# Kernel optimization log

Hardware: AMD Instinct MI355X
Metric: run time of the kernel (lower is better)

Reference implementation:

```python
import jax, jax.numpy as jnp
import numpy as np

N = 100000
E = 1600000
D = 64
EPS = 1e-5


def setup_inputs() -> dict:
    key = jax.random.key(0)
    ks = jax.random.split(key, 16)
    x = jax.random.normal(ks[0], (N, D), dtype=jnp.float32)
    edge_index = jax.random.randint(ks[1], (2, E), 0, N, dtype=jnp.int64)
    s = 1.0 / np.sqrt(D)
    params = {
        'W1': jax.random.uniform(ks[2], (D, D), jnp.float32, -s, s),
        'b1': jnp.zeros((D,), jnp.float32),
        'g1': jnp.ones((D,), jnp.float32),
        'be1': jnp.zeros((D,), jnp.float32),
        'W2': jax.random.uniform(ks[3], (D, D), jnp.float32, -s, s),
        'b2': jnp.zeros((D,), jnp.float32),
        'g2': jnp.ones((D,), jnp.float32),
        'be2': jnp.zeros((D,), jnp.float32),
        'W3': jax.random.uniform(ks[4], (D, D), jnp.float32, -s, s),
        'b3': jnp.zeros((D,), jnp.float32),
    }
    return {'x': x, 'edge_index': edge_index, **params}


def _gcn_norm(edge_index):
    # add self-loops, symmetric normalization (PyG GCNConv default)
    loop = jnp.arange(N, dtype=edge_index.dtype)
    src = jnp.concatenate([edge_index[0], loop])  # [E+N]
    dst = jnp.concatenate([edge_index[1], loop])
    deg = jax.ops.segment_sum(jnp.ones_like(src, dtype=jnp.float32), dst, num_segments=N)
    dinv = jnp.where(deg > 0, jax.lax.rsqrt(deg), 0.0)
    norm = dinv[src] * dinv[dst]  # [E+N]
    return src, dst, norm


def _gcn_conv(x, src, dst, norm, W, b):
    h = x @ W                        # [N, D] transform first (PyG order)
    msg = h[src] * norm[:, None]     # gather + scale  [E+N, D]
    out = jax.ops.segment_sum(msg, dst, num_segments=N)  # scatter-add
    return out + b


def _bn(x, g, b):
    # BatchNorm1d over nodes, batch statistics (training-mode math)
    m = jnp.mean(x, axis=0)
    v = jnp.var(x, axis=0)
    return g * (x - m) * jax.lax.rsqrt(v + EPS) + b


def reference(x, edge_index, W1, b1, g1, be1, W2, b2, g2, be2, W3, b3):
    src, dst, norm = _gcn_norm(edge_index)
    h = _gcn_conv(x, src, dst, norm, W1, b1)
    h = jax.nn.relu(_bn(h, g1, be1))
    h = _gcn_conv(h, src, dst, norm, W2, b2)
    h = jax.nn.relu(_bn(h, g2, be2))
    h = _gcn_conv(h, src, dst, norm, W3, b3)
    return h
```

## Files before the change

### kernel.cpp

```cpp
#include <hip/hip_runtime.h>
#include <hip/hip_bf16.h>


#define FD 64
#define EPSF 1e-5f

#define NBUCK 256
#define BSHIFT 9
#define BWID 512
#define SLOTS 28
#define P1_EDGES 4096
#define RPMASK 0x3FFFFF

typedef __attribute__((ext_vector_type(8))) short bf16x8;
typedef __attribute__((ext_vector_type(4))) float f32x4;

__device__ __forceinline__ ushort f2bf_bits(float f) {
  __hip_bfloat16 h = __float2bfloat16(f);
  return *(ushort*)&h;
}
__device__ __forceinline__ unsigned packbf(float lo, float hi) {
  return (unsigned)f2bf_bits(lo) | ((unsigned)f2bf_bits(hi) << 16);
}

__global__ __launch_bounds__(256) void init_kernel(int* __restrict__ bcur,
                                                   float* __restrict__ stats1,
                                                   float* __restrict__ stats2,
                                                   int nB, int cap) {
  int t = threadIdx.x;
  if (t < nB) bcur[t] = t * cap;
  if (t < 128) {
    stats1[t] = 0.f;
    stats2[t] = 0.f;
  }
}

__global__ __launch_bounds__(256) void fill1_kernel(const int* __restrict__ ei, int E,
                                                    int* __restrict__ bcur,
                                                    int2* __restrict__ stage) {
  __shared__ int2 sbuf[NBUCK][SLOTS];
  __shared__ int scnt[NBUCK];
  __shared__ int sbase[NBUCK];
  __shared__ int s_is64;
  const int tid = threadIdx.x;
  scnt[tid] = 0;
  if (tid < 64) {
    int v = ei[2 * tid + 1];
    unsigned long long nz = __ballot(v != 0);
    if (tid == 0) s_is64 = (nz == 0ull) ? 1 : 0;
  }
  __syncthreads();
  const int is64 = s_is64;
  const int base = blockIdx.x * P1_EDGES;
#pragma unroll 1
  for (int k = 0; k < P1_EDGES / 256; ++k) {
    int e = base + k * 256 + tid;
    if (e < E) {
      int s = is64 ? ei[2 * e] : ei[e];
      int d = is64 ? ei[2 * (E + e)] : ei[E + e];
      int b = d >> BSHIFT;
      int pos = atomicAdd(&scnt[b], 1);
      if (pos < SLOTS) {
        sbuf[b][pos] = make_int2(s, d);
      } else {
        stage[atomicAdd(&bcur[b], 1)] = make_int2(s, d);
      }
    }
  }
  __syncthreads();
  {
    int c = scnt[tid];
    if (c > SLOTS) c = SLOTS;
    scnt[tid] = c;
    sbase[tid] = c ? atomicAdd(&bcur[tid], c) : 0;
  }
  __syncthreads();
  for (int idx = tid; idx < NBUCK * SLOTS; idx += 256) {
    int b = idx / SLOTS, sl = idx - b * SLOTS;
    if (sl < scnt[b]) stage[sbase[b] + sl] = sbuf[b][sl];
  }
}

__global__ __launch_bounds__(256) void degscan_kernel(const int2* __restrict__ stage,
                                                      const int* __restrict__ bcur,
                                                      int* __restrict__ rowptr,
                                                      float* __restrict__ dinv,
                                                      int N, int cap) {
  __shared__ int h[BWID];
  __shared__ int ps[256];
  const int b = blockIdx.x;
  const int tid = threadIdx.x;
  h[tid] = 0;
  h[tid + 256] = 0;
  __syncthreads();
  const int lo = b * cap, hi = bcur[b];
  for (int i = lo + tid; i < hi; i += 256)
    atomicAdd(&h[stage[i].y - (b << BSHIFT)], 1);
  __syncthreads();
  const int a0 = h[2 * tid], a1 = h[2 * tid + 1];
  ps[tid] = a0 + a1;
  __syncthreads();
  for (int off = 1; off < 256; off <<= 1) {
    int v = (tid >= off) ? ps[tid - off] : 0;
    __syncthreads();
    ps[tid] += v;
    __syncthreads();
  }
  const int excl = ps[tid] - (a0 + a1);
  const int n0 = b << BSHIFT;
  const int na = n0 + 2 * tid;
  const int nb2 = na + 1;
  if (na < N) {
    rowptr[na] = (lo + excl) | (min(a0, 1023) << 22);
    dinv[na] = rsqrtf((float)(a0 + 1));
  }
  if (nb2 < N) {
    rowptr[nb2] = (lo + excl + a0) | (min(a1, 1023) << 22);
    dinv[nb2] = rsqrtf((float)(a1 + 1));
  }
}

__global__ __launch_bounds__(512) void fill2_kernel(const int2* __restrict__ stage,
                                                    const int* __restrict__ bcur,
                                                    const int* __restrict__ rowptr,
                                                    const float* __restrict__ dinv,
                                                    int2* __restrict__ colw, int N,
                                                    int cap) {
  __shared__ int lcur[BWID];
  const int b = blockIdx.x;
  const int tid = threadIdx.x;
  const int n0 = b << BSHIFT;
  if (tid < BWID) {
    int node = n0 + tid;
    lcur[tid] = (node < N) ? (rowptr[node] & RPMASK) : 0;
  }
  __syncthreads();
  const int lo = b * cap, hi = bcur[b];
  for (int i = lo + tid; i < hi; i += 512) {
    int2 sd = stage[i];
    int slot = atomicAdd(&lcur[sd.y - n0], 1);
    colw[slot] = make_int2(sd.x, __float_as_int(dinv[sd.x] * dinv[sd.y]));
  }
}

__global__ void detect64_kernel(const int* __restrict__ ei, int* __restrict__ flag) {
  int lane = threadIdx.x;
  int v = ei[2 * lane + 1];
  unsigned long long nz = __ballot(v != 0);
  if (lane == 0) *flag = (nz == 0ull) ? 1 : 0;
}
__global__ __launch_bounds__(256) void deg_atomic_kernel(const int* __restrict__ ei, int E,
                                                         const int* __restrict__ flag,
                                                         int* __restrict__ deg) {
  int e = blockIdx.x * 256 + threadIdx.x;
  if (e >= E) return;
  const int is64 = *flag;
  int d = is64 ? ei[2 * (E + e)] : ei[E + e];
  atomicAdd(&deg[d], 1);
}
__global__ __launch_bounds__(256) void dinv_kernel(const int* __restrict__ deg,
                                                   float* __restrict__ dinv, int N) {
  int i = blockIdx.x * 256 + threadIdx.x;
  if (i < N) dinv[i] = rsqrtf((float)(deg[i] + 1));
}
__global__ __launch_bounds__(1024) void scan1_kernel(const int* __restrict__ deg,
                                                     int* __restrict__ tmp,
                                                     int* __restrict__ partial, int N) {
  __shared__ int lds[1024];
  int i = blockIdx.x * 1024 + threadIdx.x;
  int v = (i < N) ? deg[i] : 0;
  lds[threadIdx.x] = v;
  __syncthreads();
  for (int off = 1; off < 1024; off <<= 1) {
    int t = (threadIdx.x >= (unsigned)off) ? lds[threadIdx.x - off] : 0;
    __syncthreads();
    lds[threadIdx.x] += t;
    __syncthreads();
  }
  if (i < N) tmp[i] = lds[threadIdx.x];
  if (threadIdx.x == 1023) partial[blockIdx.x] = lds[1023];
}
__global__ __launch_bounds__(128) void scan2_kernel(int* __restrict__ partial, int B) {
  __shared__ int lds[128];
  int t = threadIdx.x;
  int v = (t < B) ? partial[t] : 0;
  lds[t] = v;
  __syncthreads();
  for (int off = 1; off < 128; off <<= 1) {
    int tv = (t >= off) ? lds[t - off] : 0;
    __syncthreads();
    lds[t] += tv;
    __syncthreads();
  }
  if (t < B) partial[t] = lds[t] - v;
}
__global__ __launch_bounds__(1024) void scan3_kernel(const int* __restrict__ deg,
                                                     const int* __restrict__ tmp,
                                                     const int* __restrict__ partial,
                                                     int* __restrict__ rowptr,
                                                     int* __restrict__ cursor, int N) {
  int i = blockIdx.x * 1024 + threadIdx.x;
  if (i < N) {
    int d = deg[i];
    int start = tmp[i] + partial[blockIdx.x] - d;
    rowptr[i] = start | (min(d, 1023) << 22);
    cursor[i] = start;
  }
}
__global__ __launch_bounds__(256) void fill_direct_kernel(const int* __restrict__ ei, int E,
                                                          const int* __restrict__ flag,
                                                          const float* __restrict__ dinv,
                                                          int* __restrict__ cursor,
                                                          int2* __restrict__ colw) {
  int e = blockIdx.x * 256 + threadIdx.x;
  if (e >= E) return;
  const int is64 = *flag;
  int s = is64 ? ei[2 * e] : ei[e];
  int d = is64 ? ei[2 * (E + e)] : ei[E + e];
  int slot = atomicAdd(&cursor[d], 1);
  colw[slot] = make_int2(s, __float_as_int(dinv[s] * dinv[d]));
}

__global__ __launch_bounds__(256) void cast_kernel(const float* __restrict__ in,
                                                   ushort* __restrict__ out, int total) {
  int i = (blockIdx.x * 256 + threadIdx.x) * 4;
  if (i >= total) return;
  float4 v = *(const float4*)(in + i);
  ushort4 o;
  o.x = f2bf_bits(v.x);
  o.y = f2bf_bits(v.y);
  o.z = f2bf_bits(v.z);
  o.w = f2bf_bits(v.w);
  *(ushort4*)(out + i) = o;
}

__global__ __launch_bounds__(256) void bnrelu_kernel(ushort* __restrict__ T,
                                                     const float* __restrict__ stats,
                                                     const float* __restrict__ g,
                                                     const float* __restrict__ be,
                                                     int N) {
  __shared__ float sa[FD], sc[FD];
  if (threadIdx.x < FD) {
    const float invN = 1.0f / (float)N;
    float m = stats[threadIdx.x] * invN;
    float v = stats[FD + threadIdx.x] * invN - m * m;
    float r = rsqrtf(v + EPSF);
    float a = g[threadIdx.x] * r;
    sa[threadIdx.x] = a;
    sc[threadIdx.x] = be[threadIdx.x] - m * a;
  }
  __syncthreads();
  const int idx = (blockIdx.x * 256 + threadIdx.x) * 8;
  if (idx >= N * FD) return;
  const int f0 = idx & (FD - 1);
  uint4 v = *(const uint4*)(T + idx);
  float h0 = __uint_as_float(v.x << 16);
  float h1 = __uint_as_float(v.x & 0xffff0000u);
  float h2 = __uint_as_float(v.y << 16);
  float h3 = __uint_as_float(v.y & 0xffff0000u);
  float h4 = __uint_as_float(v.z << 16);
  float h5 = __uint_as_float(v.z & 0xffff0000u);
  float h6 = __uint_as_float(v.w << 16);
  float h7 = __uint_as_float(v.w & 0xffff0000u);
  h0 = fmaxf(fmaf(sa[f0 + 0], h0, sc[f0 + 0]), 0.f);
  h1 = fmaxf(fmaf(sa[f0 + 1], h1, sc[f0 + 1]), 0.f);
  h2 = fmaxf(fmaf(sa[f0 + 2], h2, sc[f0 + 2]), 0.f);
  h3 = fmaxf(fmaf(sa[f0 + 3], h3, sc[f0 + 3]), 0.f);
  h4 = fmaxf(fmaf(sa[f0 + 4], h4, sc[f0 + 4]), 0.f);
  h5 = fmaxf(fmaf(sa[f0 + 5], h5, sc[f0 + 5]), 0.f);
  h6 = fmaxf(fmaf(sa[f0 + 6], h6, sc[f0 + 6]), 0.f);
  h7 = fmaxf(fmaf(sa[f0 + 7], h7, sc[f0 + 7]), 0.f);
  uint4 o;
  o.x = packbf(h0, h1);
  o.y = packbf(h2, h3);
  o.z = packbf(h4, h5);
  o.w = packbf(h6, h7);
  *(uint4*)(T + idx) = o;
}

__global__ __launch_bounds__(256) void agg_kernel(const ushort* __restrict__ H,
                                                  const int* __restrict__ rowptr,
                                                  const int2* __restrict__ colw,
                                                  const float* __restrict__ dinv,
                                                  ushort* __restrict__ out, int N) {
  const int lane = threadIdx.x & 63;
  const int wid = threadIdx.x >> 6;
  const int grp = lane >> 4;
  const int sg = (lane >> 3) & 1;
  const int fl8 = lane & 7;
  const int dst = (blockIdx.x * 4 + wid) * 4 + grp;
  const bool live = dst < N;
  const int dc = live ? dst : N - 1;

  const unsigned rp = (unsigned)rowptr[dc];
  const int e0 = (int)(rp & RPMASK);
  const int e1 = live ? e0 + (int)(rp >> 22) : e0;

  float acc[4][8];
#pragma unroll
  for (int u = 0; u < 4; ++u)
#pragma unroll
    for (int j = 0; j < 8; ++j) acc[u][j] = 0.f;

  for (int base = e0; __any(base < e1); base += 8) {
#pragma unroll
    for (int u = 0; u < 4; ++u) {
      const int ee = base + 2 * u + sg;
      const bool valid = ee < e1;
      const int idx = valid ? ee : 0;
      const int2 cw = colw[idx];
      const float w = valid ? __int_as_float(cw.y) : 0.f;
      const uint4 uv = *(const uint4*)(H + (size_t)cw.x * FD + fl8 * 8);
      acc[u][0] = fmaf(w, __uint_as_float(uv.x << 16), acc[u][0]);
      acc[u][1] = fmaf(w, __uint_as_float(uv.x & 0xffff0000u), acc[u][1]);
      acc[u][2] = fmaf(w, __uint_as_float(uv.y << 16), acc[u][2]);
      acc[u][3] = fmaf(w, __uint_as_float(uv.y & 0xffff0000u), acc[u][3]);
      acc[u][4] = fmaf(w, __uint_as_float(uv.z << 16), acc[u][4]);
      acc[u][5] = fmaf(w, __uint_as_float(uv.z & 0xffff0000u), acc[u][5]);
      acc[u][6] = fmaf(w, __uint_as_float(uv.w << 16), acc[u][6]);
      acc[u][7] = fmaf(w, __uint_as_float(uv.w & 0xffff0000u), acc[u][7]);
    }
  }

  float r[8];
#pragma unroll
  for (int j = 0; j < 8; ++j)
    r[j] = (acc[0][j] + acc[1][j]) + (acc[2][j] + acc[3][j]);
#pragma unroll
  for (int j = 0; j < 8; ++j) r[j] += __shfl_xor(r[j], 8);

  const float di = dinv[dc];
  const float dsq = di * di;
  const uint4 sv = *(const uint4*)(H + (size_t)dc * FD + fl8 * 8);
  r[0] = fmaf(dsq, __uint_as_float(sv.x << 16), r[0]);
  r[1] = fmaf(dsq, __uint_as_float(sv.x & 0xffff0000u), r[1]);
  r[2] = fmaf(dsq, __uint_as_float(sv.y << 16), r[2]);
  r[3] = fmaf(dsq, __uint_as_float(sv.y & 0xffff0000u), r[3]);
  r[4] = fmaf(dsq, __uint_as_float(sv.z << 16), r[4]);
  r[5] = fmaf(dsq, __uint_as_float(sv.z & 0xffff0000u), r[5]);
  r[6] = fmaf(dsq, __uint_as_float(sv.w << 16), r[6]);
  r[7] = fmaf(dsq, __uint_as_float(sv.w & 0xffff0000u), r[7]);

  if (live && sg == 0) {
    uint4 o;
    o.x = packbf(r[0], r[1]);
    o.y = packbf(r[2], r[3]);
    o.z = packbf(r[4], r[5]);
    o.w = packbf(r[6], r[7]);
    *(uint4*)(out + (size_t)dst * FD + fl8 * 8) = o;
  }
}

template <bool BF16OUT>
__global__ __launch_bounds__(256) void gemm_mfma_kernel(const ushort* __restrict__ A,
                                                        const float* __restrict__ W,
                                                        const float* __restrict__ bias,
                                                        ushort* __restrict__ outb,
                                                        float* __restrict__ outf,
                                                        float* __restrict__ stats, int N) {
  const int lane = threadIdx.x & 63;
  const int wid = threadIdx.x >> 6;
  const int lo = lane & 15;
  const int hi = lane >> 4;

  __shared__ float sred[128];
  if (BF16OUT) {
    if (threadIdx.x < 128) sred[threadIdx.x] = 0.f;
    __syncthreads();
  }

  bf16x8 bfrag[2][4];
#pragma unroll
  for (int kk = 0; kk < 2; ++kk)
#pragma unroll
    for (int nt = 0; nt < 4; ++nt)
#pragma unroll
      for (int j = 0; j < 8; ++j) {
        int k = kk * 32 + hi * 8 + j;
        bfrag[kk][nt][j] = (short)f2bf_bits(W[k * FD + nt * 16 + lo]);
      }

  float bl[4];
#pragma unroll
  for (int nt = 0; nt < 4; ++nt) bl[nt] = bias[nt * 16 + lo];

  float s1[4] = {0.f, 0.f, 0.f, 0.f};
  float s2[4] = {0.f, 0.f, 0.f, 0.f};

  const int TILES = (N + 15) / 16;
  const int stride = gridDim.x * 4;
  for (int tile = blockIdx.x * 4 + wid; tile < TILES; tile += stride) {
    const int row0 = tile * 16;
    const int ar = min(row0 + lo, N - 1);
    const ushort* ap = A + (size_t)ar * FD + hi * 8;
    bf16x8 a0 = *(const bf16x8*)ap;
    bf16x8 a1 = *(const bf16x8*)(ap + 32);

    f32x4 acc[4] = {{0.f, 0.f, 0.f, 0.f},
                    {0.f, 0.f, 0.f, 0.f},
                    {0.f, 0.f, 0.f, 0.f},
                    {0.f, 0.f, 0.f, 0.f}};
#pragma unroll
    for (int nt = 0; nt < 4; ++nt) {
      acc[nt] = __builtin_amdgcn_mfma_f32_16x16x32_bf16(a0, bfrag[0][nt], acc[nt], 0, 0, 0);
      acc[nt] = __builtin_amdgcn_mfma_f32_16x16x32_bf16(a1, bfrag[1][nt], acc[nt], 0, 0, 0);
    }

#pragma unroll
    for (int nt = 0; nt < 4; ++nt) {
#pragma unroll
      for (int r = 0; r < 4; ++r) {
        int row = row0 + hi * 4 + r;
        if (row < N) {
          float o = acc[nt][r] + bl[nt];
          if (BF16OUT) {
            outb[(size_t)row * FD + nt * 16 + lo] = f2bf_bits(o);
            s1[nt] += o;
            s2[nt] += o * o;
          } else {
            outf[(size_t)row * FD + nt * 16 + lo] = o;
          }
        }
      }
    }
  }

  if (BF16OUT) {
#pragma unroll
    for (int nt = 0; nt < 4; ++nt) {
      atomicAdd(&sred[nt * 16 + lo], s1[nt]);
      atomicAdd(&sred[64 + nt * 16 + lo], s2[nt]);
    }
    __syncthreads();
    if (threadIdx.x < 128) atomicAdd(&stats[threadIdx.x], sred[threadIdx.x]);
  }
}

extern "C" void kernel_launch(void* const* d_in, const int* in_sizes, int n_in,
                              void* d_out, int out_size, void* d_ws, size_t ws_size,
                              hipStream_t stream) {
  const float* x = (const float*)d_in[0];
  const int* ei = (const int*)d_in[1];
  const float* W1 = (const float*)d_in[2];
  const float* b1 = (const float*)d_in[3];
  const float* g1 = (const float*)d_in[4];
  const float* be1 = (const float*)d_in[5];
  const float* W2 = (const float*)d_in[6];
  const float* b2 = (const float*)d_in[7];
  const float* g2 = (const float*)d_in[8];
  const float* be2 = (const float*)d_in[9];
  const float* W3 = (const float*)d_in[10];
  const float* b3 = (const float*)d_in[11];

  const int N = in_sizes[0] / FD;
  const int E = in_sizes[1] / 2;
  const int nB = (N + BWID - 1) >> BSHIFT;
  const int cap = E / nB + 1024;

  char* p = (char*)d_ws;
  auto alloc = [&](size_t bytes) {
    char* r = p;
    p += (bytes + 255) & ~(size_t)255;
    return r;
  };
  float* stats1 = (float*)alloc(128 * 4);
  float* stats2 = (float*)alloc(128 * 4);
  int* flag = (int*)alloc(4);
  int* partial = (int*)alloc(128 * 4);
  int* bcur = (int*)alloc(NBUCK * 4);
  int* deg = (int*)alloc((size_t)N * 4);
  int* tmp = (int*)alloc((size_t)N * 4);
  float* dinv = (float*)alloc((size_t)N * 4);
  int* rowptr = (int*)alloc((size_t)(N + 1) * 4);
  int* cursor = (int*)alloc((size_t)N * 4);
  int2* colw = (int2*)alloc((size_t)nB * cap * 8);
  ushort* T0 = (ushort*)alloc((size_t)N * FD * 2);
  ushort* T1 = (ushort*)alloc((size_t)N * FD * 2);
  int2* stage = (int2*)alloc((size_t)nB * cap * 8);
  size_t full_need = (size_t)(p - (char*)d_ws);
  const bool two_phase =
      ((ws_size == 0) || (ws_size >= full_need)) && (N <= NBUCK * BWID) &&
      ((size_t)nB * cap < (1u << 22));

  const int NB = (N + 1023) / 1024;
  const int EB = (E + P1_EDGES - 1) / P1_EDGES;

  if (two_phase) {
    init_kernel<<<1, 256, 0, stream>>>(bcur, stats1, stats2, nB, cap);
    fill1_kernel<<<EB, 256, 0, stream>>>(ei, E, bcur, stage);
    degscan_kernel<<<nB, 256, 0, stream>>>(stage, bcur, rowptr, dinv, N, cap);
    fill2_kernel<<<nB, 512, 0, stream>>>(stage, bcur, rowptr, dinv, colw, N, cap);
  } else {
    hipMemsetAsync(deg, 0, (size_t)N * 4, stream);
    hipMemsetAsync(stats1, 0, 128 * 4, stream);
    hipMemsetAsync(stats2, 0, 128 * 4, stream);
    detect64_kernel<<<1, 64, 0, stream>>>(ei, flag);
    deg_atomic_kernel<<<(E + 255) / 256, 256, 0, stream>>>(ei, E, flag, deg);
    dinv_kernel<<<(N + 255) / 256, 256, 0, stream>>>(deg, dinv, N);
    scan1_kernel<<<NB, 1024, 0, stream>>>(deg, tmp, partial, N);
    scan2_kernel<<<1, 128, 0, stream>>>(partial, NB);
    scan3_kernel<<<NB, 1024, 0, stream>>>(deg, tmp, partial, rowptr, cursor, N);
    fill_direct_kernel<<<(E + 255) / 256, 256, 0, stream>>>(ei, E, flag, dinv, cursor,
                                                            colw);
  }

  const int aggGrid = (N + 15) / 16;
  const int castGrid = (N * FD / 4 + 255) / 256;
  const int bnGrid = (N * FD / 8 + 255) / 256;
  const int TILES = (N + 15) / 16;
  const int gemmGrid = (TILES + 7) / 8;

  cast_kernel<<<castGrid, 256, 0, stream>>>(x, T0, N * FD);
  agg_kernel<<<aggGrid, 256, 0, stream>>>(T0, rowptr, colw, dinv, T1, N);
  gemm_mfma_kernel<true><<<gemmGrid, 256, 0, stream>>>(T1, W1, b1, T0, nullptr, stats1, N);

  bnrelu_kernel<<<bnGrid, 256, 0, stream>>>(T0, stats1, g1, be1, N);
  agg_kernel<<<aggGrid, 256, 0, stream>>>(T0, rowptr, colw, dinv, T1, N);
  gemm_mfma_kernel<true><<<gemmGrid, 256, 0, stream>>>(T1, W2, b2, T0, nullptr, stats2, N);

  bnrelu_kernel<<<bnGrid, 256, 0, stream>>>(T0, stats2, g2, be2, N);
  agg_kernel<<<aggGrid, 256, 0, stream>>>(T0, rowptr, colw, dinv, T1, N);
  gemm_mfma_kernel<false><<<gemmGrid, 256, 0, stream>>>(T1, W3, b3, nullptr,
                                                        (float*)d_out, nullptr, N);
}
```

Measured before the change: 286.9 us.

## Fuse aggregation with MFMA GEMM and pack staged edges into 32-bit words

The separate aggregation and GEMM kernels are merged. Each 16-row block aggregates neighbours into an LDS tile, then runs a 16x16x32 bf16 MFMA per wave against W, writing the output and accumulating the BN statistics. This removes the intermediate N×64 bf16 round trip and three kernel launches. Staged edges are also packed as a source index plus a local destination in 32 bits, which halves staging traffic but limits the two-phase path to N ≤ 2^17. In exchange, every block now converts W to bf16 fragments and issues one stats atomic per block, which adds work per block.

Result: slower. 475.3 us (+65.7%).

```diff
diff --git a/kernel.cpp b/kernel.cpp
--- a/kernel.cpp
+++ b/kernel.cpp
@@ -11,6 +11,7 @@
 #define SLOTS 28
 #define P1_EDGES 4096
 #define RPMASK 0x3FFFFF
+#define SMASK 0x1FFFF
 
 typedef __attribute__((ext_vector_type(8))) short bf16x8;
 typedef __attribute__((ext_vector_type(4))) float f32x4;
@@ -37,8 +38,8 @@
 
 __global__ __launch_bounds__(256) void fill1_kernel(const int* __restrict__ ei, int E,
                                                     int* __restrict__ bcur,
-                                                    int2* __restrict__ stage) {
-  __shared__ int2 sbuf[NBUCK][SLOTS];
+                                                    int* __restrict__ stage) {
+  __shared__ int sbuf[NBUCK][SLOTS];
   __shared__ int scnt[NBUCK];
   __shared__ int sbase[NBUCK];
   __shared__ int s_is64;
@@ -59,11 +60,12 @@
       int s = is64 ? ei[2 * e] : ei[e];
       int d = is64 ? ei[2 * (E + e)] : ei[E + e];
       int b = d >> BSHIFT;
+      int pk = s | ((d & (BWID - 1)) << 17);
       int pos = atomicAdd(&scnt[b], 1);
       if (pos < SLOTS) {
-        sbuf[b][pos] = make_int2(s, d);
+        sbuf[b][pos] = pk;
       } else {
-        stage[atomicAdd(&bcur[b], 1)] = make_int2(s, d);
+        stage[atomicAdd(&bcur[b], 1)] = pk;
       }
     }
   }
@@ -81,7 +83,7 @@
   }
 }
 
-__global__ __launch_bounds__(256) void degscan_kernel(const int2* __restrict__ stage,
+__global__ __launch_bounds__(256) void degscan_kernel(const int* __restrict__ stage,
                                                       const int* __restrict__ bcur,
                                                       int* __restrict__ rowptr,
                                                       float* __restrict__ dinv,
@@ -95,7 +97,7 @@
   __syncthreads();
   const int lo = b * cap, hi = bcur[b];
   for (int i = lo + tid; i < hi; i += 256)
-    atomicAdd(&h[stage[i].y - (b << BSHIFT)], 1);
+    atomicAdd(&h[(unsigned)stage[i] >> 17], 1);
   __syncthreads();
   const int a0 = h[2 * tid], a1 = h[2 * tid + 1];
   ps[tid] = a0 + a1;
@@ -120,7 +122,7 @@
   }
 }
 
-__global__ __launch_bounds__(512) void fill2_kernel(const int2* __restrict__ stage,
+__global__ __launch_bounds__(512) void fill2_kernel(const int* __restrict__ stage,
                                                     const int* __restrict__ bcur,
                                                     const int* __restrict__ rowptr,
                                                     const float* __restrict__ dinv,
@@ -137,9 +139,11 @@
   __syncthreads();
   const int lo = b * cap, hi = bcur[b];
   for (int i = lo + tid; i < hi; i += 512) {
-    int2 sd = stage[i];
-    int slot = atomicAdd(&lcur[sd.y - n0], 1);
-    colw[slot] = make_int2(sd.x, __float_as_int(dinv[sd.x] * dinv[sd.y]));
+    int pk = stage[i];
+    int s = pk & SMASK;
+    int dl = (unsigned)pk >> 17;
+    int slot = atomicAdd(&lcur[dl], 1);
+    colw[slot] = make_int2(s, __float_as_int(dinv[s] * dinv[n0 + dl]));
   }
 }
 
@@ -278,17 +282,37 @@
   *(uint4*)(T + idx) = o;
 }
 
-__global__ __launch_bounds__(256) void agg_kernel(const ushort* __restrict__ H,
-                                                  const int* __restrict__ rowptr,
-                                                  const int2* __restrict__ colw,
-                                                  const float* __restrict__ dinv,
-                                                  ushort* __restrict__ out, int N) {
-  const int lane = threadIdx.x & 63;
-  const int wid = threadIdx.x >> 6;
-  const int grp = lane >> 4;
+template <bool BF16OUT>
+__global__ __launch_bounds__(256) void fusedagg_kernel(
+    const ushort* __restrict__ H, const int* __restrict__ rowptr,
+    const int2* __restrict__ colw, const float* __restrict__ dinv,
+    const float* __restrict__ W, const float* __restrict__ bias,
+    ushort* __restrict__ outb, float* __restrict__ outf,
+    float* __restrict__ stats, int N) {
+  __shared__ ushort atile[16][72];
+  __shared__ float sred[128];
+  const int tid = threadIdx.x;
+  const int lane = tid & 63;
+  const int wid = tid >> 6;
+  const int lo = lane & 15;
+  const int hi = lane >> 4;
+  if (BF16OUT && tid < 128) sred[tid] = 0.f;
+
+  bf16x8 bfrag[2];
+#pragma unroll
+  for (int kk = 0; kk < 2; ++kk)
+#pragma unroll
+    for (int j = 0; j < 8; ++j) {
+      int k = kk * 32 + hi * 8 + j;
+      bfrag[kk][j] = (short)f2bf_bits(W[k * FD + wid * 16 + lo]);
+    }
+  const float bl = bias[wid * 16 + lo];
+
+  const int grp = hi;
   const int sg = (lane >> 3) & 1;
   const int fl8 = lane & 7;
-  const int dst = (blockIdx.x * 4 + wid) * 4 + grp;
+  const int row0 = blockIdx.x * 16;
+  const int dst = row0 + wid * 4 + grp;
   const bool live = dst < N;
   const int dc = live ? dst : N - 1;
 
@@ -341,98 +365,47 @@
   r[6] = fmaf(dsq, __uint_as_float(sv.w << 16), r[6]);
   r[7] = fmaf(dsq, __uint_as_float(sv.w & 0xffff0000u), r[7]);
 
-  if (live && sg == 0) {
+  if (sg == 0) {
+    const int dl = wid * 4 + grp;
     uint4 o;
-    o.x = packbf(r[0], r[1]);
-    o.y = packbf(r[2], r[3]);
-    o.z = packbf(r[4], r[5]);
-    o.w = packbf(r[6], r[7]);
-    *(uint4*)(out + (size_t)dst * FD + fl8 * 8) = o;
-  }
-}
-
-template <bool BF16OUT>
-__global__ __launch_bounds__(256) void gemm_mfma_kernel(const ushort* __restrict__ A,
-                                                        const float* __restrict__ W,
-                                                        const float* __restrict__ bias,
-                                                        ushort* __restrict__ outb,
-                                                        float* __restrict__ outf,
-                                                        float* __restrict__ stats, int N) {
-  const int lane = threadIdx.x & 63;
-  const int wid = threadIdx.x >> 6;
-  const int lo = lane & 15;
-  const int hi = lane >> 4;
-
-  __shared__ float sred[128];
-  if (BF16OUT) {
-    if (threadIdx.x < 128) sred[threadIdx.x] = 0.f;
-    __syncthreads();
-  }
-
-  bf16x8 bfrag[2][4];
-#pragma unroll
-  for (int kk = 0; kk < 2; ++kk)
-#pragma unroll
-    for (int nt = 0; nt < 4; ++nt)
-#pragma unroll
-      for (int j = 0; j < 8; ++j) {
-        int k = kk * 32 + hi * 8 + j;
-        bfrag[kk][nt][j] = (short)f2bf_bits(W[k * FD + nt * 16 + lo]);
-      }
-
-  float bl[4];
-#pragma unroll
-  for (int nt = 0; nt < 4; ++nt) bl[nt] = bias[nt * 16 + lo];
-
-  float s1[4] = {0.f, 0.f, 0.f, 0.f};
-  float s2[4] = {0.f, 0.f, 0.f, 0.f};
-
-  const int TILES = (N + 15) / 16;
-  const int stride = gridDim.x * 4;
-  for (int tile = blockIdx.x * 4 + wid; tile < TILES; tile += stride) {
-    const int row0 = tile * 16;
-    const int ar = min(row0 + lo, N - 1);
-    const ushort* ap = A + (size_t)ar * FD + hi * 8;
-    bf16x8 a0 = *(const bf16x8*)ap;
-    bf16x8 a1 = *(const bf16x8*)(ap + 32);
-
-    f32x4 acc[4] = {{0.f, 0.f, 0.f, 0.f},
-                    {0.f, 0.f, 0.f, 0.f},
-                    {0.f, 0.f, 0.f, 0.f},
-                    {0.f, 0.f, 0.f, 0.f}};
-#pragma unroll
-    for (int nt = 0; nt < 4; ++nt) {
-      acc[nt] = __builtin_amdgcn_mfma_f32_16x16x32_bf16(a0, bfrag[0][nt], acc[nt], 0, 0, 0);
-      acc[nt] = __builtin_amdgcn_mfma_f32_16x16x32_bf16(a1, bfrag[1][nt], acc[nt], 0, 0, 0);
+    if (live) {
+      o.x = packbf(r[0], r[1]);
+      o.y = packbf(r[2], r[3]);
+      o.z = packbf(r[4], r[5]);
+      o.w = packbf(r[6], r[7]);
+    } else {
+      o = make_uint4(0u, 0u, 0u, 0u);
     }
-
-#pragma unroll
-    for (int nt = 0; nt < 4; ++nt) {
-#pragma unroll
-      for (int r = 0; r < 4; ++r) {
-        int row = row0 + hi * 4 + r;
-        if (row < N) {
-          float o = acc[nt][r] + bl[nt];
-          if (BF16OUT) {
-            outb[(size_t)row * FD + nt * 16 + lo] = f2bf_bits(o);
-            s1[nt] += o;
-            s2[nt] += o * o;
-          } else {
-            outf[(size_t)row * FD + nt * 16 + lo] = o;
-          }
-        }
+    *(uint4*)&atile[dl][fl8 * 8] = o;
+  }
+  __syncthreads();
+
+  bf16x8 a0 = *(const bf16x8*)&atile[lo][hi * 8];
+  bf16x8 a1 = *(const bf16x8*)&atile[lo][hi * 8 + 32];
+  f32x4 oacc = {0.f, 0.f, 0.f, 0.f};
+  oacc = __builtin_amdgcn_mfma_f32_16x16x32_bf16(a0, bfrag[0], oacc, 0, 0, 0);
+  oacc = __builtin_amdgcn_mfma_f32_16x16x32_bf16(a1, bfrag[1], oacc, 0, 0, 0);
+
+  float s1 = 0.f, s2 = 0.f;
+#pragma unroll
+  for (int rg = 0; rg < 4; ++rg) {
+    int row = row0 + hi * 4 + rg;
+    if (row < N) {
+      float o = oacc[rg] + bl;
+      if (BF16OUT) {
+        outb[(size_t)row * FD + wid * 16 + lo] = f2bf_bits(o);
+        s1 += o;
+        s2 += o * o;
+      } else {
+        outf[(size_t)row * FD + wid * 16 + lo] = o;
       }
     }
   }
-
   if (BF16OUT) {
-#pragma unroll
-    for (int nt = 0; nt < 4; ++nt) {
-      atomicAdd(&sred[nt * 16 + lo], s1[nt]);
-      atomicAdd(&sred[64 + nt * 16 + lo], s2[nt]);
-    }
-    __syncthreads();
-    if (threadIdx.x < 128) atomicAdd(&stats[threadIdx.x], sred[threadIdx.x]);
+    atomicAdd(&sred[wid * 16 + lo], s1);
+    atomicAdd(&sred[64 + wid * 16 + lo], s2);
+    __syncthreads();
+    if (tid < 128) atomicAdd(&stats[tid], sred[tid]);
   }
 }
 
@@ -474,13 +447,13 @@
   int* rowptr = (int*)alloc((size_t)(N + 1) * 4);
   int* cursor = (int*)alloc((size_t)N * 4);
   int2* colw = (int2*)alloc((size_t)nB * cap * 8);
-  ushort* T0 = (ushort*)alloc((size_t)N * FD * 2);
-  ushort* T1 = (ushort*)alloc((size_t)N * FD * 2);
-  int2* stage = (int2*)alloc((size_t)nB * cap * 8);
+  ushort* TA = (ushort*)alloc((size_t)N * FD * 2);
+  ushort* TB = (ushort*)alloc((size_t)N * FD * 2);
+  int* stage = (int*)alloc((size_t)nB * cap * 4);
   size_t full_need = (size_t)(p - (char*)d_ws);
   const bool two_phase =
       ((ws_size == 0) || (ws_size >= full_need)) && (N <= NBUCK * BWID) &&
-      ((size_t)nB * cap < (1u << 22));
+      (N <= (1 << 17)) && ((size_t)nB * cap < (1u << 22));
 
   const int NB = (N + 1023) / 1024;
   const int EB = (E + P1_EDGES - 1) / P1_EDGES;
@@ -504,22 +477,18 @@
                                                             colw);
   }
 
-  const int aggGrid = (N + 15) / 16;
+  const int fusedGrid = (N + 15) / 16;
   const int castGrid = (N * FD / 4 + 255) / 256;
   const int bnGrid = (N * FD / 8 + 255) / 256;
-  const int TILES = (N + 15) / 16;
-  const int gemmGrid = (TILES + 7) / 8;
-
-  cast_kernel<<<castGrid, 256, 0, stream>>>(x, T0, N * FD);
-  agg_kernel<<<aggGrid, 256, 0, stream>>>(T0, rowptr, colw, dinv, T1, N);
-  gemm_mfma_kernel<true><<<gemmGrid, 256, 0, stream>>>(T1, W1, b1, T0, nullptr, stats1, N);
-
-  bnrelu_kernel<<<bnGrid, 256, 0, stream>>>(T0, stats1, g1, be1, N);
-  agg_kernel<<<aggGrid, 256, 0, stream>>>(T0, rowptr, colw, dinv, T1, N);
-  gemm_mfma_kernel<true><<<gemmGrid, 256, 0, stream>>>(T1, W2, b2, T0, nullptr, stats2, N);
-
-  bnrelu_kernel<<<bnGrid, 256, 0, stream>>>(T0, stats2, g2, be2, N);
-  agg_kernel<<<aggGrid, 256, 0, stream>>>(T0, rowptr, colw, dinv, T1, N);
-  gemm_mfma_kernel<false><<<gemmGrid, 256, 0, stream>>>(T1, W3, b3, nullptr,
-                                                        (float*)d_out, nullptr, N);
-}
+
+  cast_kernel<<<castGrid, 256, 0, stream>>>(x, TA, N * FD);
+  fusedagg_kernel<true><<<fusedGrid, 256, 0, stream>>>(TA, rowptr, colw, dinv, W1, b1,
+                                                       TB, nullptr, stats1, N);
+  bnrelu_kernel<<<bnGrid, 256, 0, stream>>>(TB, stats1, g1, be1, N);
+  fusedagg_kernel<true><<<fusedGrid, 256, 0, stream>>>(TB, rowptr, colw, dinv, W2, b2,
+                                                       TA, nullptr, stats2, N);
+  bnrelu_kernel<<<bnGrid, 256, 0, stream>>>(TA, stats2, g2, be2, N);
+  fusedagg_kernel<false><<<fusedGrid, 256, 0, stream>>>(TA, rowptr, colw, dinv, W3, b3,
+                                                        nullptr, (float*)d_out, nullptr,
+                                                        N);
+}
```
